# Optimization experiments

Hardware: AMD Instinct MI355X
Metric: run time of the kernel (lower is better)

## Reference

```python
import jax, jax.numpy as jnp
import numpy as np

_BIG = 1e4  # kornia uses 1e4 as the 'infinity' for masked-out kernel positions


def _windows(img, pad_val):
    """Return the 9 shifted 3x3 neighborhoods of img, stacked on axis 0.
    img: [B,C,H,W] -> [9,B,C,H,W]. Border padded with pad_val so padded
    pixels never win the min (erosion) / max (dilation), matching kornia.
    """
    B, C, H, W = img.shape
    p = jnp.pad(img, ((0, 0), (0, 0), (1, 1), (1, 1)), constant_values=pad_val)
    return jnp.stack([p[..., i:i + H, j:j + W]
                      for i in range(3) for j in range(3)], axis=0)


def _erosion(img, mask):
    w = _windows(img, _BIG)
    return jnp.min(jnp.where(mask, w, _BIG), axis=0)


def _dilation(img, mask):
    w = _windows(img, -_BIG)
    return jnp.max(jnp.where(mask, w, -_BIG), axis=0)


def setup_inputs() -> dict:
    key = jax.random.key(0)
    img = jax.random.uniform(key, (8, 3, 1024, 1024), dtype=jnp.float32)
    # kernel0: symmetric 3x3 cross structuring element
    kernel = jnp.array([[0, 1, 0], [1, 1, 1], [0, 1, 0]], dtype=jnp.int32)
    return {"img": img, "kernel": kernel}


def reference(img, kernel):
    # morphological opening = erosion followed by dilation, same structuring element
    mask = (kernel.reshape(9, 1, 1, 1, 1) == 1)
    eroded = _erosion(img, mask)
    opened = _dilation(eroded, mask)
    return opened
```

## Files before the change

### kernel.cpp

```cpp
#include <hip/hip_runtime.h>

#define BIGV 1e4f

constexpr int TW = 128;
constexpr int TH = 16;

__global__ __launch_bounds__(256) void opening_kernel(
    const float* __restrict__ img, const int* __restrict__ kern,
    float* __restrict__ out, int H, int W)
{
    __shared__ float s_img[TH + 4][TW + 4];
    __shared__ float s_ero[TH + 2][TW + 2];

    const int tid   = threadIdx.x;
    const int x0    = blockIdx.x * TW;
    const int y0    = blockIdx.y * TH;
    const size_t pbase = (size_t)blockIdx.z * H * W;

    bool m[9];
#pragma unroll
    for (int k = 0; k < 9; ++k) m[k] = (kern[k] == 1);

    for (int idx = tid; idx < (TH + 4) * (TW + 4); idx += 256) {
        int r  = idx / (TW + 4);
        int c  = idx % (TW + 4);
        int gy = y0 - 2 + r;
        int gx = x0 - 2 + c;
        float v = BIGV;
        if (gy >= 0 && gy < H && gx >= 0 && gx < W)
            v = img[pbase + (size_t)gy * W + gx];
        s_img[r][c] = v;
    }
    __syncthreads();

    for (int idx = tid; idx < (TH + 2) * (TW + 2); idx += 256) {
        int r  = idx / (TW + 2);
        int c  = idx % (TW + 2);
        int gy = y0 - 1 + r;
        int gx = x0 - 1 + c;
        float e = -BIGV;
        if (gy >= 0 && gy < H && gx >= 0 && gx < W) {
            e = BIGV;
#pragma unroll
            for (int k = 0; k < 9; ++k) {
                const int di = k / 3, dj = k % 3;
                float v = s_img[r + di][c + dj];
                e = fminf(e, m[k] ? v : BIGV);
            }
        }
        s_ero[r][c] = e;
    }
    __syncthreads();

    for (int idx = tid; idx < TH * TW; idx += 256) {
        int r = idx >> 7;
        int c = idx & (TW - 1);
        float d = -BIGV;
#pragma unroll
        for (int k = 0; k < 9; ++k) {
            const int di = k / 3, dj = k % 3;
            float v = s_ero[r + di][c + dj];
            d = fmaxf(d, m[k] ? v : -BIGV);
        }
        int gy = y0 + r, gx = x0 + c;
        if (gy < H && gx < W)
            out[pbase + (size_t)gy * W + gx] = d;
    }
}

extern "C" void kernel_launch(void* const* d_in, const int* in_sizes, int n_in,
                              void* d_out, int out_size, void* d_ws, size_t ws_size,
                              hipStream_t stream) {
    const float* img  = (const float*)d_in[0];
    const int*   kern = (const int*)d_in[1];
    float*       out  = (float*)d_out;

    const int H = 1024, W = 1024;
    const int planes = in_sizes[0] / (H * W);

    dim3 block(256);
    dim3 grid((W + TW - 1) / TW, (H + TH - 1) / TH, planes);
    opening_kernel<<<grid, block, 0, stream>>>(img, kern, out, H, W);
}
```

Before: 213.5 us.

## Replace shared-memory tiles with register rolling-row stencil and specialized cross path

Drops the two-stage shared-memory tiling and instead has each thread own four adjacent columns and walk down sixteen rows. It keeps a rolling window of input rows and eroded rows in registers, loaded with float4/float2 vector reads. A runtime check on the structuring element picks a specialized cross-shaped min3/max3 path, with a generic masked path as fallback. This removes LDS traffic and barriers and cuts redundant compares. In exchange, the halo rows and columns are re-read from global memory by neighbouring threads, and the grid assumes W and H are multiples of the tile sizes.

After: 183.4 us. -14.1%, faster.

```diff
diff --git a/kernel.cpp b/kernel.cpp
--- a/kernel.cpp
+++ b/kernel.cpp
@@ -2,70 +2,176 @@
 
 #define BIGV 1e4f
 
-constexpr int TW = 128;
-constexpr int TH = 16;
+constexpr int RH = 16;
+constexpr int TY = 4;
+
+struct Row { float2 L; float4 M; float2 R; };
+struct Ero { float eL; float4 eM; float eR; };
+
+__device__ __forceinline__ float min3f(float a, float b, float c) { return fminf(fminf(a, b), c); }
+__device__ __forceinline__ float max3f(float a, float b, float c) { return fmaxf(fmaxf(a, b), c); }
+
+__device__ __forceinline__ Row load_row(const float* __restrict__ p,
+                                        int y, int gx, int H, int W) {
+    Row r;
+    if (y >= 0 && y < H) {
+        const float* q = p + (size_t)y * W;
+        r.M = *(const float4*)(q + gx);
+        if (gx > 0)      r.L = *(const float2*)(q + gx - 2);
+        else             r.L = make_float2(BIGV, BIGV);
+        if (gx + 4 < W)  r.R = *(const float2*)(q + gx + 4);
+        else             r.R = make_float2(BIGV, BIGV);
+    } else {
+        r.L = make_float2(BIGV, BIGV);
+        r.M = make_float4(BIGV, BIGV, BIGV, BIGV);
+        r.R = make_float2(BIGV, BIGV);
+    }
+    return r;
+}
+
+__device__ __forceinline__ float rget(const Row& r, int q) {
+    switch (q) {
+        case -2: return r.L.x; case -1: return r.L.y;
+        case 0:  return r.M.x; case 1:  return r.M.y;
+        case 2:  return r.M.z; case 3:  return r.M.w;
+        case 4:  return r.R.x; default: return r.R.y;
+    }
+}
+__device__ __forceinline__ float eget(const Ero& e, int q) {
+    switch (q) {
+        case -1: return e.eL;
+        case 0:  return e.eM.x; case 1:  return e.eM.y;
+        case 2:  return e.eM.z; case 3:  return e.eM.w;
+        default: return e.eR;
+    }
+}
+
+__device__ __forceinline__ Ero erode_cross(const Row& a, const Row& b, const Row& c,
+                                           int r, int H, int gx, int W) {
+    Ero e;
+    if (r >= 0 && r < H) {
+        float vL = min3f(a.L.y, b.L.y, c.L.y);
+        float v0 = min3f(a.M.x, b.M.x, c.M.x);
+        float v1 = min3f(a.M.y, b.M.y, c.M.y);
+        float v2 = min3f(a.M.z, b.M.z, c.M.z);
+        float v3 = min3f(a.M.w, b.M.w, c.M.w);
+        float vR = min3f(a.R.x, b.R.x, c.R.x);
+        e.eL   = min3f(vL, b.L.x, b.M.x);
+        e.eM.x = min3f(v0, b.L.y, b.M.y);
+        e.eM.y = min3f(v1, b.M.x, b.M.z);
+        e.eM.z = min3f(v2, b.M.y, b.M.w);
+        e.eM.w = min3f(v3, b.M.z, b.R.x);
+        e.eR   = min3f(vR, b.M.w, b.R.y);
+        if (gx == 0)     e.eL = -BIGV;
+        if (gx + 4 >= W) e.eR = -BIGV;
+    } else {
+        e.eL = -BIGV; e.eM = make_float4(-BIGV, -BIGV, -BIGV, -BIGV); e.eR = -BIGV;
+    }
+    return e;
+}
+
+__device__ __forceinline__ float4 dilate_cross(const Ero& t, const Ero& m, const Ero& b) {
+    float vx = max3f(t.eM.x, m.eM.x, b.eM.x);
+    float vy = max3f(t.eM.y, m.eM.y, b.eM.y);
+    float vz = max3f(t.eM.z, m.eM.z, b.eM.z);
+    float vw = max3f(t.eM.w, m.eM.w, b.eM.w);
+    float4 o;
+    o.x = max3f(vx, m.eL,   m.eM.y);
+    o.y = max3f(vy, m.eM.x, m.eM.z);
+    o.z = max3f(vz, m.eM.y, m.eM.w);
+    o.w = max3f(vw, m.eM.z, m.eR);
+    return o;
+}
+
+__device__ __forceinline__ Ero erode_gen(const Row& a, const Row& b, const Row& c,
+                                         const bool* m, int r, int H, int gx, int W) {
+    Ero e;
+    if (r >= 0 && r < H) {
+        float v[6];
+#pragma unroll
+        for (int p = 0; p < 6; ++p) {
+            float acc = BIGV;
+#pragma unroll
+            for (int k = 0; k < 9; ++k) {
+                const int di = k / 3, dj = k % 3;
+                const Row& rr = (di == 0) ? a : ((di == 1) ? b : c);
+                float t = rget(rr, p - 2 + dj);
+                acc = fminf(acc, m[k] ? t : BIGV);
+            }
+            v[p] = acc;
+        }
+        e.eL = v[0]; e.eM.x = v[1]; e.eM.y = v[2]; e.eM.z = v[3]; e.eM.w = v[4]; e.eR = v[5];
+        if (gx == 0)     e.eL = -BIGV;
+        if (gx + 4 >= W) e.eR = -BIGV;
+    } else {
+        e.eL = -BIGV; e.eM = make_float4(-BIGV, -BIGV, -BIGV, -BIGV); e.eR = -BIGV;
+    }
+    return e;
+}
+
+__device__ __forceinline__ float4 dilate_gen(const Ero& e0, const Ero& e1, const Ero& e2,
+                                             const bool* m) {
+    float o[4];
+#pragma unroll
+    for (int j = 0; j < 4; ++j) {
+        float acc = -BIGV;
+#pragma unroll
+        for (int k = 0; k < 9; ++k) {
+            const int di = k / 3, dj = k % 3;
+            const Ero& ee = (di == 0) ? e0 : ((di == 1) ? e1 : e2);
+            float t = eget(ee, j + dj - 1);
+            acc = fmaxf(acc, m[k] ? t : -BIGV);
+        }
+        o[j] = acc;
+    }
+    return make_float4(o[0], o[1], o[2], o[3]);
+}
+
+template <bool CROSS>
+__device__ __forceinline__ void run(const float* __restrict__ img, float* __restrict__ out,
+                                    const bool* m, int gx, int y0, int H, int W) {
+    Row B = load_row(img, y0 - 2, gx, H, W);
+    Row C = load_row(img, y0 - 1, gx, H, W);
+    Row D = load_row(img, y0,     gx, H, W);
+    Ero E0 = CROSS ? erode_cross(B, C, D, y0 - 1, H, gx, W)
+                   : erode_gen(B, C, D, m, y0 - 1, H, gx, W);
+    C = D;
+    Row Cc = load_row(img, y0,     gx, H, W);
+    Row Dd = load_row(img, y0 + 1, gx, H, W);
+    Ero E1 = CROSS ? erode_cross(load_row(img, y0 - 1, gx, H, W), Cc, Dd, y0, H, gx, W)
+                   : erode_gen(load_row(img, y0 - 1, gx, H, W), Cc, Dd, m, y0, H, gx, W);
+#pragma unroll
+    for (int i = 0; i < RH; ++i) {
+        const int y = y0 + i;
+        Row N = load_row(img, y + 2, gx, H, W);
+        Ero E2 = CROSS ? erode_cross(Cc, Dd, N, y + 1, H, gx, W)
+                       : erode_gen(Cc, Dd, N, m, y + 1, H, gx, W);
+        float4 o = CROSS ? dilate_cross(E0, E1, E2) : dilate_gen(E0, E1, E2, m);
+        *(float4*)(out + (size_t)y * W + gx) = o;
+        Cc = Dd; Dd = N;
+        E0 = E1; E1 = E2;
+    }
+}
 
 __global__ __launch_bounds__(256) void opening_kernel(
     const float* __restrict__ img, const int* __restrict__ kern,
     float* __restrict__ out, int H, int W)
 {
-    __shared__ float s_img[TH + 4][TW + 4];
-    __shared__ float s_ero[TH + 2][TW + 2];
-
-    const int tid   = threadIdx.x;
-    const int x0    = blockIdx.x * TW;
-    const int y0    = blockIdx.y * TH;
+    const int lx = threadIdx.x & 63;
+    const int ty = threadIdx.x >> 6;
+    const int gx = blockIdx.x * 256 + lx * 4;
+    const int y0 = (blockIdx.y * TY + ty) * RH;
     const size_t pbase = (size_t)blockIdx.z * H * W;
 
     bool m[9];
 #pragma unroll
     for (int k = 0; k < 9; ++k) m[k] = (kern[k] == 1);
 
-    for (int idx = tid; idx < (TH + 4) * (TW + 4); idx += 256) {
-        int r  = idx / (TW + 4);
-        int c  = idx % (TW + 4);
-        int gy = y0 - 2 + r;
-        int gx = x0 - 2 + c;
-        float v = BIGV;
-        if (gy >= 0 && gy < H && gx >= 0 && gx < W)
-            v = img[pbase + (size_t)gy * W + gx];
-        s_img[r][c] = v;
-    }
-    __syncthreads();
+    const bool cross = m[1] && m[3] && m[4] && m[5] && m[7] &&
+                       !m[0] && !m[2] && !m[6] && !m[8];
 
-    for (int idx = tid; idx < (TH + 2) * (TW + 2); idx += 256) {
-        int r  = idx / (TW + 2);
-        int c  = idx % (TW + 2);
-        int gy = y0 - 1 + r;
-        int gx = x0 - 1 + c;
-        float e = -BIGV;
-        if (gy >= 0 && gy < H && gx >= 0 && gx < W) {
-            e = BIGV;
-#pragma unroll
-            for (int k = 0; k < 9; ++k) {
-                const int di = k / 3, dj = k % 3;
-                float v = s_img[r + di][c + dj];
-                e = fminf(e, m[k] ? v : BIGV);
-            }
-        }
-        s_ero[r][c] = e;
-    }
-    __syncthreads();
-
-    for (int idx = tid; idx < TH * TW; idx += 256) {
-        int r = idx >> 7;
-        int c = idx & (TW - 1);
-        float d = -BIGV;
-#pragma unroll
-        for (int k = 0; k < 9; ++k) {
-            const int di = k / 3, dj = k % 3;
-            float v = s_ero[r + di][c + dj];
-            d = fmaxf(d, m[k] ? v : -BIGV);
-        }
-        int gy = y0 + r, gx = x0 + c;
-        if (gy < H && gx < W)
-            out[pbase + (size_t)gy * W + gx] = d;
-    }
+    if (cross) run<true >(img + pbase, out + pbase, m, gx, y0, H, W);
+    else       run<false>(img + pbase, out + pbase, m, gx, y0, H, W);
 }
 
 extern "C" void kernel_launch(void* const* d_in, const int* in_sizes, int n_in,
@@ -79,6 +185,6 @@
     const int planes = in_sizes[0] / (H * W);
 
     dim3 block(256);
-    dim3 grid((W + TW - 1) / TW, (H + TH - 1) / TH, planes);
+    dim3 grid(W / 256, H / (TY * RH), planes);
     opening_kernel<<<grid, block, 0, stream>>>(img, kern, out, H, W);
 }
```

## Stream full-width row bands through an LDS ring with rolling register erosion

Applied to the files above, without the earlier changes.

Replaces the 2D 128x16 tile kernel with blocks that each own a 16-row band across the full 1024-wide row. Rows are staged into a 16-slot LDS ring buffer with async global_load_lds, and each thread handles 4 columns with float4 reads. Erosion rows are rolled through registers and fed straight into the dilation, so there is no intermediate shared buffer and far less halo overfetch. A runtime check on the kernel values picks a specialized path with min3/max3 for the cross structuring element, and a general masked path is kept for any other kernel. The cost is more LDS per block and a reliance on correct ordering between the async loads and the barriers.

Result: faster. 184.2 us (-13.7%).

```diff
diff --git a/kernel.cpp b/kernel.cpp
--- a/kernel.cpp
+++ b/kernel.cpp
@@ -1,70 +1,159 @@
 #include <hip/hip_runtime.h>
+#include <stdint.h>
 
 #define BIGV 1e4f
 
-constexpr int TW = 128;
-constexpr int TH = 16;
+constexpr int W     = 1024;
+constexpr int TH    = 4;
+constexpr int CPB   = 4;
+constexpr int NSLOT = 16;
+
+typedef const __attribute__((address_space(1))) uint32_t glb_u32;
+typedef __attribute__((address_space(3)))       uint32_t lds_u32;
+
+__device__ __forceinline__ float min3f(float a, float b, float c) { return fminf(fminf(a, b), c); }
+__device__ __forceinline__ float max3f(float a, float b, float c) { return fmaxf(fmaxf(a, b), c); }
+
+__device__ __forceinline__ void stage_row(const float* __restrict__ plane, int y, int ly,
+                                          float* smem, int lane, int H) {
+    float* dst = smem + (size_t)(ly & (NSLOT - 1)) * W;
+    if (y >= 0 && y < H) {
+        const float* src = plane + (size_t)y * W + lane * 4;
+#pragma unroll
+        for (int seg = 0; seg < 4; ++seg)
+            __builtin_amdgcn_global_load_lds((glb_u32*)(src + seg * 256),
+                                             (lds_u32*)(dst + seg * 256), 16, 0, 0);
+    } else {
+        const float4 pad = make_float4(BIGV, BIGV, BIGV, BIGV);
+#pragma unroll
+        for (int seg = 0; seg < 4; ++seg)
+            *(float4*)(dst + seg * 256 + lane * 4) = pad;
+    }
+}
+
+struct T3 { float4 a, b, c; };
+__device__ __forceinline__ T3 read_row(const float* smem, int ly, int tid) {
+    const float4* p = (const float4*)(smem + (size_t)(ly & (NSLOT - 1)) * W);
+    T3 t;
+    t.b = p[tid];
+    t.a = (tid > 0)       ? p[tid - 1] : make_float4(BIGV, BIGV, BIGV, BIGV);
+    t.c = (tid < W/4 - 1) ? p[tid + 1] : make_float4(BIGV, BIGV, BIGV, BIGV);
+    return t;
+}
+__device__ __forceinline__ float tg(const T3& t, int i) {
+    switch (i) {
+        case 0:  return t.a.x; case 1:  return t.a.y; case 2:  return t.a.z; case 3:  return t.a.w;
+        case 4:  return t.b.x; case 5:  return t.b.y; case 6:  return t.b.z; case 7:  return t.b.w;
+        case 8:  return t.c.x; case 9:  return t.c.y; case 10: return t.c.z; default: return t.c.w;
+    }
+}
+
+struct E6 { float e[6]; };
+
+template <bool CROSS>
+__device__ __forceinline__ E6 ero_row(const T3& A, const T3& B, const T3& C,
+                                      const bool* m, int y, int H, int x) {
+    E6 e;
+    if (y >= 0 && y < H) {
+#pragma unroll
+        for (int j = 0; j < 6; ++j) {
+            if (CROSS) {
+                float v = min3f(tg(A, 3 + j), tg(B, 3 + j), tg(C, 3 + j));
+                e.e[j] = min3f(v, tg(B, 2 + j), tg(B, 4 + j));
+            } else {
+                float acc = BIGV;
+#pragma unroll
+                for (int k = 0; k < 9; ++k) {
+                    const int di = k / 3, dj = k % 3;
+                    const T3& r = (di == 0) ? A : ((di == 1) ? B : C);
+                    acc = fminf(acc, m[k] ? tg(r, 2 + j + dj) : BIGV);
+                }
+                e.e[j] = acc;
+            }
+        }
+        if (x == 0)     e.e[0] = -BIGV;
+        if (x == W - 4) e.e[5] = -BIGV;
+    } else {
+#pragma unroll
+        for (int j = 0; j < 6; ++j) e.e[j] = -BIGV;
+    }
+    return e;
+}
+
+template <bool CROSS>
+__device__ __forceinline__ float4 dil_row(const E6& t, const E6& md, const E6& b,
+                                          const bool* m) {
+    float o[4];
+#pragma unroll
+    for (int j = 0; j < 4; ++j) {
+        if (CROSS) {
+            float v = max3f(t.e[j + 1], md.e[j + 1], b.e[j + 1]);
+            o[j] = max3f(v, md.e[j], md.e[j + 2]);
+        } else {
+            float acc = -BIGV;
+#pragma unroll
+            for (int k = 0; k < 9; ++k) {
+                const int di = k / 3, dj = k % 3;
+                const E6& ee = (di == 0) ? t : ((di == 1) ? md : b);
+                acc = fmaxf(acc, m[k] ? ee.e[j + dj] : -BIGV);
+            }
+            o[j] = acc;
+        }
+    }
+    return make_float4(o[0], o[1], o[2], o[3]);
+}
+
+template <bool CROSS>
+__device__ __forceinline__ void compute_chunk(const float* smem, float* __restrict__ outp,
+                                              const bool* m, int yy, int ly0, int tid, int H) {
+    const int x = tid * 4;
+    T3 A = read_row(smem, ly0 - 2, tid);
+    T3 B = read_row(smem, ly0 - 1, tid);
+    T3 C = read_row(smem, ly0,     tid);
+    E6 E0 = ero_row<CROSS>(A, B, C, m, yy - 1, H, x);
+    T3 D = read_row(smem, ly0 + 1, tid);
+    E6 E1 = ero_row<CROSS>(B, C, D, m, yy, H, x);
+#pragma unroll
+    for (int i = 0; i < TH; ++i) {
+        T3 N = read_row(smem, ly0 + 2 + i, tid);
+        E6 E2 = ero_row<CROSS>(C, D, N, m, yy + 1 + i, H, x);
+        float4 o = dil_row<CROSS>(E0, E1, E2, m);
+        *(float4*)(outp + (size_t)(yy + i) * W + x) = o;
+        C = D; D = N;
+        E0 = E1; E1 = E2;
+    }
+}
 
 __global__ __launch_bounds__(256) void opening_kernel(
     const float* __restrict__ img, const int* __restrict__ kern,
-    float* __restrict__ out, int H, int W)
+    float* __restrict__ out, int H)
 {
-    __shared__ float s_img[TH + 4][TW + 4];
-    __shared__ float s_ero[TH + 2][TW + 2];
+    __shared__ float smem[NSLOT * W];
 
-    const int tid   = threadIdx.x;
-    const int x0    = blockIdx.x * TW;
-    const int y0    = blockIdx.y * TH;
-    const size_t pbase = (size_t)blockIdx.z * H * W;
+    const int tid  = threadIdx.x;
+    const int wv   = tid >> 6;
+    const int lane = tid & 63;
+    const int y0   = blockIdx.x * (TH * CPB);
+    const size_t pb = (size_t)blockIdx.y * H * W;
+    const float* ip = img + pb;
+    float*       op = out + pb;
 
     bool m[9];
 #pragma unroll
     for (int k = 0; k < 9; ++k) m[k] = (kern[k] == 1);
+    const bool cross = m[1] && m[3] && m[4] && m[5] && m[7] &&
+                       !m[0] && !m[2] && !m[6] && !m[8];
 
-    for (int idx = tid; idx < (TH + 4) * (TW + 4); idx += 256) {
-        int r  = idx / (TW + 4);
-        int c  = idx % (TW + 4);
-        int gy = y0 - 2 + r;
-        int gx = x0 - 2 + c;
-        float v = BIGV;
-        if (gy >= 0 && gy < H && gx >= 0 && gx < W)
-            v = img[pbase + (size_t)gy * W + gx];
-        s_img[r][c] = v;
-    }
-    __syncthreads();
+#pragma unroll
+    for (int j = 0; j < 3; ++j)
+        stage_row(ip, y0 - 2 + wv + 4 * j, wv + 4 * j, smem, lane, H);
 
-    for (int idx = tid; idx < (TH + 2) * (TW + 2); idx += 256) {
-        int r  = idx / (TW + 2);
-        int c  = idx % (TW + 2);
-        int gy = y0 - 1 + r;
-        int gx = x0 - 1 + c;
-        float e = -BIGV;
-        if (gy >= 0 && gy < H && gx >= 0 && gx < W) {
-            e = BIGV;
-#pragma unroll
-            for (int k = 0; k < 9; ++k) {
-                const int di = k / 3, dj = k % 3;
-                float v = s_img[r + di][c + dj];
-                e = fminf(e, m[k] ? v : BIGV);
-            }
-        }
-        s_ero[r][c] = e;
-    }
-    __syncthreads();
-
-    for (int idx = tid; idx < TH * TW; idx += 256) {
-        int r = idx >> 7;
-        int c = idx & (TW - 1);
-        float d = -BIGV;
-#pragma unroll
-        for (int k = 0; k < 9; ++k) {
-            const int di = k / 3, dj = k % 3;
-            float v = s_ero[r + di][c + dj];
-            d = fmaxf(d, m[k] ? v : -BIGV);
-        }
-        int gy = y0 + r, gx = x0 + c;
-        if (gy < H && gx < W)
-            out[pbase + (size_t)gy * W + gx] = d;
+    for (int k = 0; k < CPB; ++k) {
+        __syncthreads();
+        if (k < CPB - 2)
+            stage_row(ip, y0 + 10 + 4 * k + wv, 4 * k + 12 + wv, smem, lane, H);
+        if (cross) compute_chunk<true >(smem, op, m, y0 + TH * k, 4 * k + 2, tid, H);
+        else       compute_chunk<false>(smem, op, m, y0 + TH * k, 4 * k + 2, tid, H);
     }
 }
 
@@ -75,10 +164,10 @@
     const int*   kern = (const int*)d_in[1];
     float*       out  = (float*)d_out;
 
-    const int H = 1024, W = 1024;
+    const int H = 1024;
     const int planes = in_sizes[0] / (H * W);
 
     dim3 block(256);
-    dim3 grid((W + TW - 1) / TW, (H + TH - 1) / TH, planes);
-    opening_kernel<<<grid, block, 0, stream>>>(img, kern, out, H, W);
+    dim3 grid(H / (TH * CPB), planes);
+    opening_kernel<<<grid, block, 0, stream>>>(img, kern, out, H);
 }
```
